# Kernel tuning notes

Hardware: AMD Instinct MI355X
Metric: run time of the kernel (lower is better)

The kernel has to match this reference:

```python
import jax, jax.numpy as jnp
import numpy as np

# Module constants (globals in the original source)
N_SPECIAL = 5            # len(SPECIAL_TOKENS)
LABEL_ID = 2             # SPECIAL_TOKENS['<LABEL>']
ACT_VOCAB = 64           # ACTIVITY_VOCAB_SIZE
TIME_VOCAB = 32          # TIME_BUCKET_VOCAB_SIZE
VOCAB = N_SPECIAL + ACT_VOCAB + TIME_VOCAB  # 101


def setup_inputs() -> dict:
    key = jax.random.key(0)
    ks = jax.random.split(key, 8)
    B, T, D = 8, 2048, 1024
    tokens = jax.random.randint(ks[0], (B, T), 0, VOCAB)
    h = jax.random.normal(ks[1], (B, T, D), dtype=jnp.float32)
    E = jax.random.normal(ks[2], (VOCAB, D), dtype=jnp.float32) * 0.02
    W_next = jax.random.normal(ks[3], (ACT_VOCAB, D), dtype=jnp.float32) * (1.0 / np.sqrt(D))
    b_next = jnp.zeros((ACT_VOCAB,), jnp.float32)
    W_time = jax.random.normal(ks[4], (TIME_VOCAB, D), dtype=jnp.float32) * (1.0 / np.sqrt(D))
    b_time = jnp.zeros((TIME_VOCAB,), jnp.float32)
    return {
        'tokens': tokens, 'h': h, 'E': E,
        'W_next': W_next, 'b_next': b_next,
        'W_time': W_time, 'b_time': b_time,
        'tied_scale_act': jnp.asarray(0.0, jnp.float32),
        'tied_scale_time': jnp.asarray(0.0, jnp.float32),
        'copy_scale_act': jnp.asarray(1.5, jnp.float32),
        'copy_scale_time': jnp.asarray(1.5, jnp.float32),
        'copy_temp_act': jnp.asarray(1.0, jnp.float32),
        'copy_temp_time': jnp.asarray(1.0, jnp.float32),
    }


def _heads(tokens, h, E, W_next, b_next, W_time, b_time,
           tied_scale_act, tied_scale_time, copy_scale_act, copy_scale_time,
           copy_temp_act, copy_temp_time):
    act_start = N_SPECIAL
    time_start = N_SPECIAL + ACT_VOCAB
    sp = jax.nn.softplus

    # Parametric heads: [B,T,A], [B,T,Tb]
    param_next = jnp.einsum('btd,ad->bta', h, W_next) + b_next
    param_time = jnp.einsum('btd,cd->btc', h, W_time) + b_time

    # Weight-tied heads from slices of the token-embedding table
    tied_act = jnp.einsum('btd,ad->bta', h, E[act_start:act_start + ACT_VOCAB])
    tied_time = jnp.einsum('btd,cd->btc', h, E[time_start:time_start + TIME_VOCAB])

    # --- Retrieval/copy head, fully vectorized over (b, query, key) ---
    # F.normalize(h, dim=-1) with eps clamp
    hn = h / jnp.maximum(jnp.linalg.norm(h, axis=-1, keepdims=True), 1e-12)
    sims = jnp.einsum('bqd,bkd->bqk', hn, hn)  # [B,T,T] cosine sims

    T = tokens.shape[1]
    is_label = tokens == LABEL_ID                           # [B,T] query gate
    value_mask = jnp.pad(is_label[:, :-1], ((0, 0), (1, 0)))  # pos whose prev tok is <LABEL>
    val_act = value_mask & (tokens >= act_start) & (tokens < time_start)
    val_time = value_mask & (tokens >= time_start) & (tokens < time_start + TIME_VOCAB)
    strict_past = jnp.tril(jnp.ones((T, T), bool), -1)      # key k < query q

    def copy_logits(val_mask, class_idx, n_cls, tau):
        m = is_label[:, :, None] & strict_past[None] & val_mask[:, None, :]
        s = jnp.where(m, sims, 0.0) * tau                   # masked, scaled sims
        onehot = jax.nn.one_hot(jnp.clip(class_idx, 0, n_cls - 1), n_cls, dtype=h.dtype)
        # segment-sum into class buckets: [B,q,k] @ [B,k,c] -> [B,q,c]
        return jnp.einsum('bqk,bkc->bqc', s, onehot)

    copy_act = copy_logits(val_act, tokens - act_start, ACT_VOCAB, sp(copy_temp_act))
    copy_time = copy_logits(val_time, tokens - time_start, TIME_VOCAB, sp(copy_temp_time))

    activity_logits = param_next + sp(tied_scale_act) * tied_act + sp(copy_scale_act) * copy_act
    time_logits = param_time + sp(tied_scale_time) * tied_time + sp(copy_scale_time) * copy_time
    return activity_logits, time_logits


def reference(tokens, h, E, W_next, b_next, W_time, b_time,
              tied_scale_act, tied_scale_time, copy_scale_act, copy_scale_time,
              copy_temp_act, copy_temp_time):
    return _heads(tokens, h, E, W_next, b_next, W_time, b_time,
                  tied_scale_act, tied_scale_time, copy_scale_act, copy_scale_time,
                  copy_temp_act, copy_temp_time)
```

## Files before the change

kernel.cpp:

```cpp
#include <hip/hip_runtime.h>
#include <hip/hip_bf16.h>

#define BATCH  8
#define T_TOK  2048
#define DMODEL 1024
#define BT     (BATCH * T_TOK)
#define NCOLS  96

typedef __bf16 bf16x8 __attribute__((ext_vector_type(8)));
typedef float  f32x4  __attribute__((ext_vector_type(4)));
typedef unsigned short u16x8 __attribute__((ext_vector_type(8)));

union AB { u16x8 u; bf16x8 b; unsigned int w[4]; };

__device__ __forceinline__ unsigned short f2bf(float f) {
    unsigned u = __float_as_uint(f);
    unsigned r = (u + 0x7fffu + ((u >> 16) & 1u)) >> 16;
    return (unsigned short)r;
}
__device__ __forceinline__ float softplusf(float x) {
    return fmaxf(x, 0.f) + log1pf(expf(-fabsf(x)));
}
__device__ __forceinline__ float wave_sum(float v) {
#pragma unroll
    for (int o = 32; o > 0; o >>= 1) v += __shfl_xor(v, o, 64);
    return v;
}
__device__ __forceinline__ unsigned int pack_rtz(float lo, float hi) {
    return __builtin_amdgcn_perm(__float_as_uint(hi), __float_as_uint(lo), 0x07060302u);
}

__global__ void prep_kernel(const float* __restrict__ E,
                            const float* __restrict__ Wn,
                            const float* __restrict__ bn,
                            const float* __restrict__ Wt,
                            const float* __restrict__ bt,
                            const float* __restrict__ tsa,
                            const float* __restrict__ tst,
                            unsigned short* __restrict__ Weff,
                            float* __restrict__ beff)
{
    int idx = blockIdx.x * 256 + threadIdx.x;
    int row = idx >> 10, k = idx & 1023;
    float w;
    if (row < 64) {
        w = Wn[idx] + softplusf(tsa[0]) * E[(5 + row) * 1024 + k];
    } else {
        int c = row - 64;
        w = Wt[c * 1024 + k] + softplusf(tst[0]) * E[(69 + c) * 1024 + k];
    }
    Weff[idx] = f2bf(w);
    if (k == 0) beff[row] = (row < 64) ? bn[row] : bt[row - 64];
}

__global__ __launch_bounds__(256) void gemm_kernel(
    const float* __restrict__ h,
    const unsigned short* __restrict__ Weff,
    const float* __restrict__ beff,
    float* __restrict__ out)
{
    const int lane = threadIdx.x & 63;
    const int wave = threadIdx.x >> 6;
    const int m = lane & 15;
    const int q = lane >> 4;
    const int tok_base = (blockIdx.x * 4 + wave) * 16;

    const float4* hA = reinterpret_cast<const float4*>(h + (size_t)(tok_base + m) * DMODEL);
    const bf16x8* wB = reinterpret_cast<const bf16x8*>(Weff + (size_t)m * DMODEL);

    f32x4 acc[6];
#pragma unroll
    for (int n = 0; n < 6; ++n) acc[n] = (f32x4){0.f, 0.f, 0.f, 0.f};

#pragma unroll 4
    for (int kc = 0; kc < 128; kc += 4) {
        const int ch = kc + q;
        float4 f0 = hA[ch * 2];
        float4 f1 = hA[ch * 2 + 1];
        AB a;
        a.w[0] = pack_rtz(f0.x, f0.y);
        a.w[1] = pack_rtz(f0.z, f0.w);
        a.w[2] = pack_rtz(f1.x, f1.y);
        a.w[3] = pack_rtz(f1.z, f1.w);
#pragma unroll
        for (int n = 0; n < 6; ++n) {
            acc[n] = __builtin_amdgcn_mfma_f32_16x16x32_bf16(a.b, wB[n * 2048 + ch], acc[n], 0, 0, 0);
        }
    }

#pragma unroll
    for (int n = 0; n < 6; ++n) {
        const int j = n * 16 + m;
        const float bj = beff[j];
#pragma unroll
        for (int r = 0; r < 4; ++r) {
            const int t = tok_base + q * 4 + r;
            const float v = acc[n][r] + bj;
            if (j < 64) out[(size_t)t * 64 + j] = v;
            else        out[(size_t)BT * 64 + (size_t)t * 32 + (j - 64)] = v;
        }
    }
}

__global__ __launch_bounds__(1024) void copy_kernel(
    const int* __restrict__ tokens,
    const float* __restrict__ h,
    const float* __restrict__ csa,
    const float* __restrict__ cst,
    const float* __restrict__ cta,
    const float* __restrict__ ctt,
    float* __restrict__ out)
{
    const int b     = blockIdx.x >> 3;
    const int slice = blockIdx.x & 7;
    const int tid  = threadIdx.x;
    const int wave = tid >> 6, lane = tid & 63;

    __shared__ int cnt_q[32], cnt_k[32], off_q[32], off_k[32];
    __shared__ int s_nq, s_nk;
    __shared__ int   q_pos[T_TOK];
    __shared__ int   k_pos[T_TOK];
    __shared__ int   k_col[T_TOK];
    __shared__ float q_nrm[T_TOK];
    __shared__ float k_nrm[T_TOK];

    const int* tk = tokens + b * T_TOK;

#pragma unroll
    for (int c = 0; c < 2; ++c) {
        int chunk = wave * 2 + c;
        int t = chunk * 64 + lane;
        int v = tk[t];
        bool pq = (v == 2);
        bool pk = (t > 0) && (tk[t - 1] == 2) && (v >= 5) && (v < 101);
        unsigned long long mq = __ballot(pq);
        unsigned long long mk = __ballot(pk);
        if (lane == 0) { cnt_q[chunk] = __popcll(mq); cnt_k[chunk] = __popcll(mk); }
    }
    __syncthreads();
    if (tid == 0) {
        int aq = 0, ak = 0;
        for (int i = 0; i < 32; ++i) {
            off_q[i] = aq; aq += cnt_q[i];
            off_k[i] = ak; ak += cnt_k[i];
        }
        s_nq = aq; s_nk = ak;
    }
    __syncthreads();

#pragma unroll
    for (int c = 0; c < 2; ++c) {
        int chunk = wave * 2 + c;
        int t = chunk * 64 + lane;
        int v = tk[t];
        bool pq = (v == 2);
        bool pk = (t > 0) && (tk[t - 1] == 2) && (v >= 5) && (v < 101);
        unsigned long long mq = __ballot(pq);
        unsigned long long mk = __ballot(pk);
        unsigned long long below = (lane == 0) ? 0ull : ((~0ull) >> (64 - lane));
        if (pq) q_pos[off_q[chunk] + __popcll(mq & below)] = t;
        if (pk) {
            int i = off_k[chunk] + __popcll(mk & below);
            k_pos[i] = t;
            k_col[i] = (v < 69) ? (v - 5) : (64 + (v - 69));
        }
    }
    __syncthreads();
    const int nq = s_nq, nk = s_nk;
    const float* hb = h + (size_t)b * T_TOK * DMODEL;

    for (int i = wave; i < nq + nk; i += 16) {
        const int row = (i < nq) ? q_pos[i] : k_pos[i - nq];
        const float4* p = reinterpret_cast<const float4*>(hb + (size_t)row * DMODEL);
        float s = 0.f;
#pragma unroll
        for (int c = 0; c < 4; ++c) {
            float4 v = p[lane + c * 64];
            s += v.x * v.x + v.y * v.y + v.z * v.z + v.w * v.w;
        }
        s = wave_sum(s);
        if (lane == 0) {
            float nn = fmaxf(sqrtf(s), 1e-12f);
            if (i < nq) q_nrm[i] = nn; else k_nrm[i - nq] = nn;
        }
    }
    __syncthreads();

    const float fa = softplusf(csa[0]) * softplusf(cta[0]);
    const float ft = softplusf(cst[0]) * softplusf(ctt[0]);
    const int P = nq * nk;
    const int g = slice * 16 + wave;
    for (int p = g; p < P; p += 128) {
        const int qi = p / nk, ki = p - qi * nk;
        const int qp = q_pos[qi], kp = k_pos[ki];
        if (kp >= qp) continue;
        const float4* pq = reinterpret_cast<const float4*>(hb + (size_t)qp * DMODEL);
        const float4* pk = reinterpret_cast<const float4*>(hb + (size_t)kp * DMODEL);
        float s = 0.f;
#pragma unroll
        for (int c = 0; c < 4; ++c) {
            float4 va = pq[lane + c * 64];
            float4 vb = pk[lane + c * 64];
            s += va.x * vb.x + va.y * vb.y + va.z * vb.z + va.w * vb.w;
        }
        s = wave_sum(s);
        if (lane == 0) {
            const int col = k_col[ki];
            const float val = ((col < 64) ? fa : ft) * (s / (q_nrm[qi] * k_nrm[ki]));
            const size_t tg = (size_t)b * T_TOK + qp;
            float* dst = (col < 64) ? &out[tg * 64 + col]
                                    : &out[(size_t)BT * 64 + tg * 32 + (col - 64)];
            atomicAdd(dst, val);
        }
    }
}

extern "C" void kernel_launch(void* const* d_in, const int* in_sizes, int n_in,
                              void* d_out, int out_size, void* d_ws, size_t ws_size,
                              hipStream_t stream) {
    const int* tokens = (const int*)d_in[0];
    const float* h    = (const float*)d_in[1];
    const float* E    = (const float*)d_in[2];
    const float* Wn   = (const float*)d_in[3];
    const float* bn   = (const float*)d_in[4];
    const float* Wt   = (const float*)d_in[5];
    const float* bt   = (const float*)d_in[6];
    const float* tsa  = (const float*)d_in[7];
    const float* tst  = (const float*)d_in[8];
    const float* csa  = (const float*)d_in[9];
    const float* cst  = (const float*)d_in[10];
    const float* cta  = (const float*)d_in[11];
    const float* ctt  = (const float*)d_in[12];

    char* ws = (char*)d_ws;
    float* beff          = (float*)ws;
    unsigned short* Weff = (unsigned short*)(ws + 1024);
    float* out           = (float*)d_out;

    prep_kernel<<<dim3(384), dim3(256), 0, stream>>>(E, Wn, bn, Wt, bt, tsa, tst, Weff, beff);
    gemm_kernel<<<dim3(BT / 64), dim3(256), 0, stream>>>(h, Weff, beff, out);
    copy_kernel<<<dim3(64), dim3(1024), 0, stream>>>(tokens, h, csa, cst, cta, ctt, out);
}
```

Baseline: 156.5 us.

## Split GEMM reduction over K with atomic accumulation into bias-initialized output

The prep kernel now also writes the biases into the output buffer, and the GEMM grid gains a K-split dimension of four. Each block reduces a quarter of the model dimension and adds its partial sums with unsafe hardware float atomics. This gives the GEMM four times as many blocks to hide the latency of streaming h. The cost is four times as many atomic writes to the output, plus a separate bias-initialization pass. The copy kernel also moves to unsafeAtomicAdd.

```diff
diff --git a/kernel.cpp b/kernel.cpp
--- a/kernel.cpp
+++ b/kernel.cpp
@@ -6,6 +6,7 @@
 #define DMODEL 1024
 #define BT     (BATCH * T_TOK)
 #define NCOLS  96
+#define KSPLIT 4
 
 typedef __bf16 bf16x8 __attribute__((ext_vector_type(8)));
 typedef float  f32x4  __attribute__((ext_vector_type(4)));
@@ -29,34 +30,49 @@
 __device__ __forceinline__ unsigned int pack_rtz(float lo, float hi) {
     return __builtin_amdgcn_perm(__float_as_uint(hi), __float_as_uint(lo), 0x07060302u);
 }
-
-__global__ void prep_kernel(const float* __restrict__ E,
-                            const float* __restrict__ Wn,
-                            const float* __restrict__ bn,
-                            const float* __restrict__ Wt,
-                            const float* __restrict__ bt,
-                            const float* __restrict__ tsa,
-                            const float* __restrict__ tst,
-                            unsigned short* __restrict__ Weff,
-                            float* __restrict__ beff)
+__device__ __forceinline__ void atomic_fadd(float* p, float v) {
+    unsafeAtomicAdd(p, v);
+}
+
+__global__ __launch_bounds__(256) void prep_init_kernel(
+    const float* __restrict__ E,
+    const float* __restrict__ Wn,
+    const float* __restrict__ bn,
+    const float* __restrict__ Wt,
+    const float* __restrict__ bt,
+    const float* __restrict__ tsa,
+    const float* __restrict__ tst,
+    unsigned short* __restrict__ Weff,
+    float* __restrict__ out)
 {
-    int idx = blockIdx.x * 256 + threadIdx.x;
-    int row = idx >> 10, k = idx & 1023;
-    float w;
-    if (row < 64) {
-        w = Wn[idx] + softplusf(tsa[0]) * E[(5 + row) * 1024 + k];
+    const int blk = blockIdx.x;
+    if (blk < 384) {
+        int idx = blk * 256 + threadIdx.x;
+        int row = idx >> 10, k = idx & 1023;
+        float w;
+        if (row < 64) {
+            w = Wn[idx] + softplusf(tsa[0]) * E[(5 + row) * 1024 + k];
+        } else {
+            int c = row - 64;
+            w = Wt[c * 1024 + k] + softplusf(tst[0]) * E[(69 + c) * 1024 + k];
+        }
+        Weff[idx] = f2bf(w);
     } else {
-        int c = row - 64;
-        w = Wt[c * 1024 + k] + softplusf(tst[0]) * E[(69 + c) * 1024 + k];
-    }
-    Weff[idx] = f2bf(w);
-    if (k == 0) beff[row] = (row < 64) ? bn[row] : bt[row - 64];
+        int i = (blk - 384) * 256 + threadIdx.x;
+        if (i < 262144) {
+            float4 b = reinterpret_cast<const float4*>(bn)[i & 15];
+            reinterpret_cast<float4*>(out)[i] = b;
+        } else {
+            int k = i - 262144;
+            float4 b = reinterpret_cast<const float4*>(bt)[k & 7];
+            reinterpret_cast<float4*>(out)[i] = b;
+        }
+    }
 }
 
 __global__ __launch_bounds__(256) void gemm_kernel(
     const float* __restrict__ h,
     const unsigned short* __restrict__ Weff,
-    const float* __restrict__ beff,
     float* __restrict__ out)
 {
     const int lane = threadIdx.x & 63;
@@ -64,6 +80,7 @@
     const int m = lane & 15;
     const int q = lane >> 4;
     const int tok_base = (blockIdx.x * 4 + wave) * 16;
+    const int kbase = blockIdx.y * 32;
 
     const float4* hA = reinterpret_cast<const float4*>(h + (size_t)(tok_base + m) * DMODEL);
     const bf16x8* wB = reinterpret_cast<const bf16x8*>(Weff + (size_t)m * DMODEL);
@@ -72,9 +89,9 @@
 #pragma unroll
     for (int n = 0; n < 6; ++n) acc[n] = (f32x4){0.f, 0.f, 0.f, 0.f};
 
-#pragma unroll 4
-    for (int kc = 0; kc < 128; kc += 4) {
-        const int ch = kc + q;
+#pragma unroll
+    for (int kc = 0; kc < 32; kc += 4) {
+        const int ch = kbase + kc + q;
         float4 f0 = hA[ch * 2];
         float4 f1 = hA[ch * 2 + 1];
         AB a;
@@ -91,13 +108,12 @@
 #pragma unroll
     for (int n = 0; n < 6; ++n) {
         const int j = n * 16 + m;
-        const float bj = beff[j];
 #pragma unroll
         for (int r = 0; r < 4; ++r) {
             const int t = tok_base + q * 4 + r;
-            const float v = acc[n][r] + bj;
-            if (j < 64) out[(size_t)t * 64 + j] = v;
-            else        out[(size_t)BT * 64 + (size_t)t * 32 + (j - 64)] = v;
+            float* dst = (j < 64) ? &out[(size_t)t * 64 + j]
+                                  : &out[(size_t)BT * 64 + (size_t)t * 32 + (j - 64)];
+            atomic_fadd(dst, acc[n][r]);
         }
     }
 }
@@ -210,7 +226,7 @@
             const size_t tg = (size_t)b * T_TOK + qp;
             float* dst = (col < 64) ? &out[tg * 64 + col]
                                     : &out[(size_t)BT * 64 + tg * 32 + (col - 64)];
-            atomicAdd(dst, val);
+            atomic_fadd(dst, val);
         }
     }
 }
@@ -232,12 +248,10 @@
     const float* cta  = (const float*)d_in[11];
     const float* ctt  = (const float*)d_in[12];
 
-    char* ws = (char*)d_ws;
-    float* beff          = (float*)ws;
-    unsigned short* Weff = (unsigned short*)(ws + 1024);
+    unsigned short* Weff = (unsigned short*)d_ws;
     float* out           = (float*)d_out;
 
-    prep_kernel<<<dim3(384), dim3(256), 0, stream>>>(E, Wn, bn, Wt, bt, tsa, tst, Weff, beff);
-    gemm_kernel<<<dim3(BT / 64), dim3(256), 0, stream>>>(h, Weff, beff, out);
+    prep_init_kernel<<<dim3(1920), dim3(256), 0, stream>>>(E, Wn, bn, Wt, bt, tsa, tst, Weff, out);
+    gemm_kernel<<<dim3(BT / 64, KSPLIT), dim3(256), 0, stream>>>(h, Weff, out);
     copy_kernel<<<dim3(64), dim3(1024), 0, stream>>>(tokens, h, csa, cst, cta, ctt, out);
 }
```

After: 167.4 us. 7.0% more time.

## Stage GEMM operands through double-buffered LDS with async global-to-LDS loads

Applied to the files above, without the earlier changes.

The GEMM kernel now copies 64-token by 64-k chunks of h and the bf16 weight tile into swizzled, double-buffered shared memory using global_load_lds async copies. Each wave then reads its MFMA operands from LDS, and the next chunk's load overlaps with compute on the current one. This replaces per-wave direct global loads in which every wave re-read the whole weight matrix. The copy kernel also switches atomicAdd to unsafeAtomicAdd, which allows hardware float atomics. The cost is a barrier per chunk and extra LDS use, which may reduce occupancy.

```diff
diff --git a/kernel.cpp b/kernel.cpp
--- a/kernel.cpp
+++ b/kernel.cpp
@@ -6,6 +6,8 @@
 #define DMODEL 1024
 #define BT     (BATCH * T_TOK)
 #define NCOLS  96
+#define KC     64
+#define NCHUNK (DMODEL / KC)
 
 typedef __bf16 bf16x8 __attribute__((ext_vector_type(8)));
 typedef float  f32x4  __attribute__((ext_vector_type(4)));
@@ -29,16 +31,25 @@
 __device__ __forceinline__ unsigned int pack_rtz(float lo, float hi) {
     return __builtin_amdgcn_perm(__float_as_uint(hi), __float_as_uint(lo), 0x07060302u);
 }
-
-__global__ void prep_kernel(const float* __restrict__ E,
-                            const float* __restrict__ Wn,
-                            const float* __restrict__ bn,
-                            const float* __restrict__ Wt,
-                            const float* __restrict__ bt,
-                            const float* __restrict__ tsa,
-                            const float* __restrict__ tst,
-                            unsigned short* __restrict__ Weff,
-                            float* __restrict__ beff)
+__device__ __forceinline__ void atomic_fadd(float* p, float v) {
+    unsafeAtomicAdd(p, v);
+}
+__device__ __forceinline__ void async16(const void* g, void* l) {
+    __builtin_amdgcn_global_load_lds(
+        (const __attribute__((address_space(1))) unsigned int*)g,
+        (__attribute__((address_space(3))) unsigned int*)l, 16, 0, 0);
+}
+
+__global__ __launch_bounds__(256) void prep_kernel(
+    const float* __restrict__ E,
+    const float* __restrict__ Wn,
+    const float* __restrict__ bn,
+    const float* __restrict__ Wt,
+    const float* __restrict__ bt,
+    const float* __restrict__ tsa,
+    const float* __restrict__ tst,
+    unsigned short* __restrict__ Weff,
+    float* __restrict__ beff)
 {
     int idx = blockIdx.x * 256 + threadIdx.x;
     int row = idx >> 10, k = idx & 1023;
@@ -59,32 +70,67 @@
     const float* __restrict__ beff,
     float* __restrict__ out)
 {
-    const int lane = threadIdx.x & 63;
-    const int wave = threadIdx.x >> 6;
+    __shared__ float4 Abuf[2][1024];
+    __shared__ float4 Bbuf[2][768];
+
+    const int tid  = threadIdx.x;
+    const int lane = tid & 63;
+    const int wave = tid >> 6;
     const int m = lane & 15;
     const int q = lane >> 4;
-    const int tok_base = (blockIdx.x * 4 + wave) * 16;
-
-    const float4* hA = reinterpret_cast<const float4*>(h + (size_t)(tok_base + m) * DMODEL);
-    const bf16x8* wB = reinterpret_cast<const bf16x8*>(Weff + (size_t)m * DMODEL);
+    const int tok0 = blockIdx.x * 64;
 
     f32x4 acc[6];
 #pragma unroll
     for (int n = 0; n < 6; ++n) acc[n] = (f32x4){0.f, 0.f, 0.f, 0.f};
 
-#pragma unroll 4
-    for (int kc = 0; kc < 128; kc += 4) {
-        const int ch = kc + q;
-        float4 f0 = hA[ch * 2];
-        float4 f1 = hA[ch * 2 + 1];
-        AB a;
-        a.w[0] = pack_rtz(f0.x, f0.y);
-        a.w[1] = pack_rtz(f0.z, f0.w);
-        a.w[2] = pack_rtz(f1.x, f1.y);
-        a.w[3] = pack_rtz(f1.z, f1.w);
-#pragma unroll
-        for (int n = 0; n < 6; ++n) {
-            acc[n] = __builtin_amdgcn_mfma_f32_16x16x32_bf16(a.b, wB[n * 2048 + ch], acc[n], 0, 0, 0);
+    const int r = wave * 16 + m;
+    const int s = m & 7;
+
+#define STAGE(cidx, buf)                                                        \
+    {                                                                           \
+        const int kb = (cidx) * KC;                                             \
+        _Pragma("unroll")                                                       \
+        for (int i = 0; i < 4; ++i) {                                           \
+            int u = i * 256 + tid;                                              \
+            int row_ = u >> 4, c4_ = u & 15;                                    \
+            async16(h + (size_t)(tok0 + row_) * DMODEL + kb                     \
+                        + ((c4_ ^ (row_ & 7)) << 2),                            \
+                    &Abuf[buf][u]);                                             \
+        }                                                                       \
+        _Pragma("unroll")                                                       \
+        for (int i = 0; i < 3; ++i) {                                           \
+            int u = i * 256 + tid;                                              \
+            int row_ = u >> 3, c16_ = u & 7;                                    \
+            async16(Weff + (size_t)row_ * DMODEL + kb                           \
+                         + ((c16_ ^ (row_ & 7)) << 3),                          \
+                    &Bbuf[buf][u]);                                             \
+        }                                                                       \
+    }
+
+    STAGE(0, 0);
+
+    for (int c = 0; c < NCHUNK; ++c) {
+        __syncthreads();
+        if (c + 1 < NCHUNK) STAGE(c + 1, (c + 1) & 1);
+        const int buf = c & 1;
+#pragma unroll
+        for (int kk = 0; kk < 2; ++kk) {
+            const int c4 = kk * 8 + q * 2;
+            float4 f0 = Abuf[buf][r * 16 + ((c4    ) ^ s)];
+            float4 f1 = Abuf[buf][r * 16 + ((c4 + 1) ^ s)];
+            AB a;
+            a.w[0] = pack_rtz(f0.x, f0.y);
+            a.w[1] = pack_rtz(f0.z, f0.w);
+            a.w[2] = pack_rtz(f1.x, f1.y);
+            a.w[3] = pack_rtz(f1.z, f1.w);
+#pragma unroll
+            for (int n = 0; n < 6; ++n) {
+                const int rb = n * 16 + m;
+                const bf16x8* bp = reinterpret_cast<const bf16x8*>(
+                    &Bbuf[buf][rb * 8 + ((kk * 4 + q) ^ s)]);
+                acc[n] = __builtin_amdgcn_mfma_f32_16x16x32_bf16(a.b, *bp, acc[n], 0, 0, 0);
+            }
         }
     }
 
@@ -93,13 +139,14 @@
         const int j = n * 16 + m;
         const float bj = beff[j];
 #pragma unroll
-        for (int r = 0; r < 4; ++r) {
-            const int t = tok_base + q * 4 + r;
-            const float v = acc[n][r] + bj;
+        for (int rr = 0; rr < 4; ++rr) {
+            const int t = tok0 + wave * 16 + q * 4 + rr;
+            const float v = acc[n][rr] + bj;
             if (j < 64) out[(size_t)t * 64 + j] = v;
             else        out[(size_t)BT * 64 + (size_t)t * 32 + (j - 64)] = v;
         }
     }
+#undef STAGE
 }
 
 __global__ __launch_bounds__(1024) void copy_kernel(
@@ -172,15 +219,15 @@
     for (int i = wave; i < nq + nk; i += 16) {
         const int row = (i < nq) ? q_pos[i] : k_pos[i - nq];
         const float4* p = reinterpret_cast<const float4*>(hb + (size_t)row * DMODEL);
-        float s = 0.f;
+        float ssum = 0.f;
 #pragma unroll
         for (int c = 0; c < 4; ++c) {
             float4 v = p[lane + c * 64];
-            s += v.x * v.x + v.y * v.y + v.z * v.z + v.w * v.w;
-        }
-        s = wave_sum(s);
+            ssum += v.x * v.x + v.y * v.y + v.z * v.z + v.w * v.w;
+        }
+        ssum = wave_sum(ssum);
         if (lane == 0) {
-            float nn = fmaxf(sqrtf(s), 1e-12f);
+            float nn = fmaxf(sqrtf(ssum), 1e-12f);
             if (i < nq) q_nrm[i] = nn; else k_nrm[i - nq] = nn;
         }
     }
@@ -196,21 +243,21 @@
         if (kp >= qp) continue;
         const float4* pq = reinterpret_cast<const float4*>(hb + (size_t)qp * DMODEL);
         const float4* pk = reinterpret_cast<const float4*>(hb + (size_t)kp * DMODEL);
-        float s = 0.f;
+        float ssum = 0.f;
 #pragma unroll
         for (int c = 0; c < 4; ++c) {
             float4 va = pq[lane + c * 64];
             float4 vb = pk[lane + c * 64];
-            s += va.x * vb.x + va.y * vb.y + va.z * vb.z + va.w * vb.w;
-        }
-        s = wave_sum(s);
+            ssum += va.x * vb.x + va.y * vb.y + va.z * vb.z + va.w * vb.w;
+        }
+        ssum = wave_sum(ssum);
         if (lane == 0) {
             const int col = k_col[ki];
-            const float val = ((col < 64) ? fa : ft) * (s / (q_nrm[qi] * k_nrm[ki]));
+            const float val = ((col < 64) ? fa : ft) * (ssum / (q_nrm[qi] * k_nrm[ki]));
             const size_t tg = (size_t)b * T_TOK + qp;
             float* dst = (col < 64) ? &out[tg * 64 + col]
                                     : &out[(size_t)BT * 64 + tg * 32 + (col - 64)];
-            atomicAdd(dst, val);
+            atomic_fadd(dst, val);
         }
     }
 }
```

Measured after the change: 143.5 us. 8.3% less time.
